# Performance work log

Hardware: AMD Instinct MI355X
Metric: run time of the kernel (lower is better)

Reference implementation:

```python
import math
import jax, jax.numpy as jnp
import numpy as np

CAPACITY_FACTOR = 1.0

def setup_inputs() -> dict:
    key = jax.random.key(0)
    k1, k2 = jax.random.split(key)
    token_input = jax.random.normal(k1, (4096, 1024), dtype=jnp.float32)
    wg2_weight = jax.random.normal(k2, (64, 1024), dtype=jnp.float32) * 0.02
    return {"token_input": token_input, "wg2_weight": wg2_weight}

def reference(token_input, wg2_weight):
    S, _ = token_input.shape
    E = wg2_weight.shape[0]
    num_2nd = E // 4
    capacity = int(2 * math.ceil(S / num_2nd) * CAPACITY_FACTOR)  # static
    eps = jnp.finfo(jnp.float32).eps

    logits = token_input @ wg2_weight.T               # [S, E]
    gates = jax.nn.softmax(logits, axis=-1)           # [S, E]

    # top-1 expert
    idx1 = jnp.argmax(gates, axis=1)                  # [S]
    mask1 = jax.nn.one_hot(idx1, E, dtype=jnp.int32)  # [S, E]

    # second expert via gumbel sampling on the gate values (masked-out top1)
    gumbel = jax.random.gumbel(jax.random.key(42), gates.shape, dtype=jnp.float32)
    noisy = gates + gumbel
    masked = jnp.where(mask1.astype(bool), -jnp.inf, noisy)
    idx2 = jnp.argmax(masked, axis=1)
    mask2 = jax.nn.one_hot(idx2, E, dtype=jnp.int32)

    # cumsum-based slot locations (fused_cumsum_sub_one)
    locations1 = jnp.cumsum(mask1, axis=0) - 1                       # [S, E]
    locations2 = jnp.cumsum(mask2, axis=0) - 1 + jnp.sum(mask1, axis=0, keepdims=True)

    # load-balance aux loss
    me = jnp.mean(gates, axis=0)
    ce = jnp.mean(mask1.astype(gates.dtype), axis=0)
    l_aux = jnp.sum(me * ce) / num_2nd * (E * E)

    # capacity dropping
    mask1 = mask1 * (locations1 < capacity).astype(jnp.int32)
    mask2 = mask2 * (locations2 < capacity).astype(jnp.int32)

    # gate probs renormalized over kept assignments
    gates1_s = jnp.sum(gates * mask1, axis=1)
    gates2_s = jnp.sum(gates * mask2, axis=1)
    denom = jnp.maximum(gates1_s + gates2_s, eps)
    gates1_s = gates1_s / denom
    gates2_s = gates2_s / denom

    loc1_s = jnp.sum(locations1 * mask1, axis=1)      # [S]
    loc2_s = jnp.sum(locations2 * mask2, axis=1)

    gates1 = gates1_s[:, None] * mask1.astype(gates.dtype)  # [S, E]
    gates2 = gates2_s[:, None] * mask2.astype(gates.dtype)

    loc1_sc = jax.nn.one_hot(loc1_s, capacity, dtype=gates.dtype)  # [S, C]
    loc2_sc = jax.nn.one_hot(loc2_s, capacity, dtype=gates.dtype)

    combine_weights = (jnp.einsum('se,sc->sec', gates1, loc1_sc)
                       + jnp.einsum('se,sc->sec', gates2, loc2_sc))  # [S, E, C]
    dispatch_mask = combine_weights > 0
    return l_aux, combine_weights, dispatch_mask
```

## Files before the change

kernel.cpp:

```cpp
#include <hip/hip_runtime.h>
#include <math.h>
#include <stdint.h>

#define S_TOK 4096
#define N_EXP 64
#define MDIM  1024
#define TB    8
#define CAP   512
#define NBLK_GATE (S_TOK / TB)

#define SEC ((size_t)S_TOK * N_EXP * CAP)


struct TokRec { int idx1; int idx2; float g1; float g2; };

__device__ __forceinline__ void tf4(uint32_t& x0, uint32_t& x1,
                                    int r0, int r1, int r2, int r3) {
  x0 += x1; x1 = (x1 << r0) | (x1 >> (32 - r0)); x1 ^= x0;
  x0 += x1; x1 = (x1 << r1) | (x1 >> (32 - r1)); x1 ^= x0;
  x0 += x1; x1 = (x1 << r2) | (x1 >> (32 - r2)); x1 ^= x0;
  x0 += x1; x1 = (x1 << r3) | (x1 >> (32 - r3)); x1 ^= x0;
}

__device__ __forceinline__ float jax_gumbel(uint32_t f) {
  const uint32_t k0 = 0u, k1 = 42u;
  const uint32_t k2 = 0x1BD11BDAu ^ 42u;
  uint32_t x0 = 0u + k0;
  uint32_t x1 = f + k1;
  tf4(x0, x1, 13, 15, 26,  6); x0 += k1; x1 += k2 + 1u;
  tf4(x0, x1, 17, 29, 16, 24); x0 += k2; x1 += k0 + 2u;
  tf4(x0, x1, 13, 15, 26,  6); x0 += k0; x1 += k1 + 3u;
  tf4(x0, x1, 17, 29, 16, 24); x0 += k1; x1 += k2 + 4u;
  tf4(x0, x1, 13, 15, 26,  6); x0 += k2; x1 += k0 + 5u;
  uint32_t bits = x0 ^ x1;
  float u = __uint_as_float((bits >> 9) | 0x3F800000u) - 1.0f;
  u = fmaxf(u, 1.17549435e-38f);
  return -logf(-logf(u));
}

__global__ __launch_bounds__(256) void k_gate(const float* __restrict__ tok,
                                              const float* __restrict__ W,
                                              TokRec* __restrict__ recs,
                                              float* __restrict__ mePart) {
  __shared__ float t_lds[TB * MDIM];
  __shared__ float logits_l[TB * N_EXP];
  __shared__ float meAcc[4][N_EXP];

  const int tid  = threadIdx.x;
  const int wave = tid >> 6;
  const int lane = tid & 63;
  const int tok0 = blockIdx.x * TB;

  {
    const float4* src = (const float4*)(tok + (size_t)tok0 * MDIM);
    float4* dst = (float4*)t_lds;
    #pragma unroll
    for (int i = 0; i < (TB * MDIM / 4) / 256; ++i)
      dst[tid + i * 256] = src[tid + i * 256];
  }
  __syncthreads();

  for (int p = 0; p < N_EXP / 4; ++p) {
    const int e = p * 4 + wave;
    const float* wr = W + (size_t)e * MDIM;
    float acc[TB];
    #pragma unroll
    for (int t = 0; t < TB; ++t) acc[t] = 0.f;
    for (int k = lane; k < MDIM; k += 64) {
      float wv = wr[k];
      #pragma unroll
      for (int t = 0; t < TB; ++t) acc[t] = fmaf(t_lds[t * MDIM + k], wv, acc[t]);
    }
    #pragma unroll
    for (int t = 0; t < TB; ++t) {
      float v = acc[t];
      #pragma unroll
      for (int o = 32; o >= 1; o >>= 1) v += __shfl_xor(v, o, 64);
      if (lane == 0) logits_l[t * N_EXP + e] = v;
    }
  }
  __syncthreads();

  const int e = lane;
  float meLocal = 0.f;
  #pragma unroll
  for (int rep = 0; rep < 2; ++rep) {
    const int t = wave + rep * 4;
    const int s = tok0 + t;
    float x = logits_l[t * N_EXP + e];
    float m = x;
    #pragma unroll
    for (int o = 32; o >= 1; o >>= 1) m = fmaxf(m, __shfl_xor(m, o, 64));
    float ex = expf(x - m);
    float sum = ex;
    #pragma unroll
    for (int o = 32; o >= 1; o >>= 1) sum += __shfl_xor(sum, o, 64);
    float gate = ex / sum;
    meLocal += gate;

    float bv = gate; int bi = e;
    #pragma unroll
    for (int o = 32; o >= 1; o >>= 1) {
      float ov = __shfl_xor(bv, o, 64);
      int   oi = __shfl_xor(bi, o, 64);
      if (ov > bv || (ov == bv && oi < bi)) { bv = ov; bi = oi; }
    }
    const int idx1 = bi;

    float noisy = (e == idx1) ? -INFINITY
                              : (gate + jax_gumbel((uint32_t)(s * N_EXP + e)));
    float bv2 = noisy; int bi2 = e;
    #pragma unroll
    for (int o = 32; o >= 1; o >>= 1) {
      float ov = __shfl_xor(bv2, o, 64);
      int   oi = __shfl_xor(bi2, o, 64);
      if (ov > bv2 || (ov == bv2 && oi < bi2)) { bv2 = ov; bi2 = oi; }
    }
    const int idx2 = bi2;

    float g1 = __shfl(gate, idx1, 64);
    float g2 = __shfl(gate, idx2, 64);
    if (lane == 0) {
      TokRec r; r.idx1 = idx1; r.idx2 = idx2; r.g1 = g1; r.g2 = g2;
      recs[s] = r;
    }
  }
  meAcc[wave][e] = meLocal;
  __syncthreads();
  if (wave == 0)
    mePart[(size_t)blockIdx.x * N_EXP + e] =
        meAcc[0][e] + meAcc[1][e] + meAcc[2][e] + meAcc[3][e];
}

__global__ __launch_bounds__(1024) void k_finish(const TokRec* __restrict__ recs,
                                                 const float* __restrict__ mePart,
                                                 float* __restrict__ out) {
  __shared__ unsigned short pk_l[S_TOK];
  __shared__ unsigned short rank1_l[S_TOK];
  __shared__ unsigned short rank2_l[S_TOK];
  __shared__ int   cnt1[16][N_EXP];
  __shared__ int   cnt2[16][N_EXP];
  __shared__ int   off1[16][N_EXP];
  __shared__ int   off2[16][N_EXP];
  __shared__ int   total1_l[N_EXP];
  __shared__ float meAcc[16][N_EXP];
  __shared__ float laux_l[N_EXP];

  const int tid  = threadIdx.x;
  const int wave = tid >> 6;
  const int lane = tid & 63;

  for (int s = tid; s < S_TOK; s += 1024) {
    TokRec r = recs[s];
    pk_l[s] = (unsigned short)(r.idx1 | (r.idx2 << 8));
  }
  __syncthreads();

  {
    int c1 = 0, c2 = 0;
    const int s0 = wave * (S_TOK / 16);
    for (int j = 0; j < S_TOK / 16; ++j) {
      const int s = s0 + j;
      const int v  = pk_l[s];
      const int v1 = v & 0xFF;
      const int v2 = v >> 8;
      if (v1 == lane) { rank1_l[s] = (unsigned short)c1; ++c1; }
      if (v2 == lane) { rank2_l[s] = (unsigned short)c2; ++c2; }
    }
    cnt1[wave][lane] = c1;
    cnt2[wave][lane] = c2;
  }
  __syncthreads();

  if (tid < N_EXP) {
    int off = 0;
    #pragma unroll
    for (int w = 0; w < 16; ++w) { off1[w][tid] = off; off += cnt1[w][tid]; }
    total1_l[tid] = off;
    int o2 = off;
    #pragma unroll
    for (int w = 0; w < 16; ++w) { off2[w][tid] = o2; o2 += cnt2[w][tid]; }
  }
  __syncthreads();

  float* comb = out + 1;
  float* mask = out + 1 + SEC;
  for (int s = tid; s < S_TOK; s += 1024) {
    TokRec r = recs[s];
    const int w  = s / (S_TOK / 16);
    const int l1 = (int)rank1_l[s] + off1[w][r.idx1];
    const int l2 = (int)rank2_l[s] + off2[w][r.idx2];
    const bool k1 = l1 < CAP;
    const bool k2 = l2 < CAP;
    float g1 = k1 ? r.g1 : 0.f;
    float g2 = k2 ? r.g2 : 0.f;
    float denom = fmaxf(g1 + g2, 1.1920929e-07f);
    float g1n = g1 / denom;
    float g2n = g2 / denom;
    const size_t base = (size_t)s * N_EXP * CAP;
    if (k1) { size_t o = base + (size_t)r.idx1 * CAP + l1; comb[o] = g1n; mask[o] = 1.0f; }
    if (k2) { size_t o = base + (size_t)r.idx2 * CAP + l2; comb[o] = g2n; mask[o] = 1.0f; }
  }

  {
    float a = 0.f;
    for (int b = wave; b < NBLK_GATE; b += 16) a += mePart[(size_t)b * N_EXP + lane];
    meAcc[wave][lane] = a;
  }
  __syncthreads();
  if (tid < N_EXP) {
    float sg = 0.f;
    #pragma unroll
    for (int w = 0; w < 16; ++w) sg += meAcc[w][tid];
    laux_l[tid] = sg * (float)total1_l[tid];
  }
  __syncthreads();
  if (tid == 0) {
    float t = 0.f;
    for (int e2 = 0; e2 < N_EXP; ++e2) t += laux_l[e2];
    out[0] = t * (1.0f / 65536.0f);
  }
}

extern "C" void kernel_launch(void* const* d_in, const int* in_sizes, int n_in,
                              void* d_out, int out_size, void* d_ws, size_t ws_size,
                              hipStream_t stream) {
  const float* tok = (const float*)d_in[0];
  const float* W   = (const float*)d_in[1];
  float* out = (float*)d_out;

  TokRec* recs   = (TokRec*)d_ws;
  float*  mePart = (float*)((char*)d_ws + S_TOK * sizeof(TokRec));

  k_gate  <<<NBLK_GATE, 256, 0, stream>>>(tok, W, recs, mePart);
  k_finish<<<1, 1024, 0, stream>>>(recs, mePart, out);
}
```

Baseline: 1.022 ms.

## Restructure gate GEMV to vectorized direct global loads without LDS staging

The gating matmul no longer stages the token tile in shared memory. Each lane now owns one of 16 experts per wave and one of 4 K-chunks, and reads weights and tokens from global memory as float4 vectors. The cross-lane reduction shrinks from six shuffle steps to two. This removes the LDS copy, the barrier and most shuffle work, but relies on cache broadcast for the token reads, which are repeated across the 16 expert lanes.

```diff
diff --git a/kernel.cpp b/kernel.cpp
--- a/kernel.cpp
+++ b/kernel.cpp
@@ -13,6 +13,8 @@
 
 
 struct TokRec { int idx1; int idx2; float g1; float g2; };
+
+typedef float f4v __attribute__((ext_vector_type(4)));
 
 __device__ __forceinline__ void tf4(uint32_t& x0, uint32_t& x1,
                                     int r0, int r1, int r2, int r3) {
@@ -42,7 +44,6 @@
                                               const float* __restrict__ W,
                                               TokRec* __restrict__ recs,
                                               float* __restrict__ mePart) {
-  __shared__ float t_lds[TB * MDIM];
   __shared__ float logits_l[TB * N_EXP];
   __shared__ float meAcc[4][N_EXP];
 
@@ -51,32 +52,36 @@
   const int lane = tid & 63;
   const int tok0 = blockIdx.x * TB;
 
+  const int e_sub = lane & 15;
+  const int kc    = lane >> 4;
+  const int eW    = wave * 16 + e_sub;
+
   {
-    const float4* src = (const float4*)(tok + (size_t)tok0 * MDIM);
-    float4* dst = (float4*)t_lds;
-    #pragma unroll
-    for (int i = 0; i < (TB * MDIM / 4) / 256; ++i)
-      dst[tid + i * 256] = src[tid + i * 256];
-  }
-  __syncthreads();
-
-  for (int p = 0; p < N_EXP / 4; ++p) {
-    const int e = p * 4 + wave;
-    const float* wr = W + (size_t)e * MDIM;
+    const f4v* wr4 = (const f4v*)(W   + (size_t)eW   * MDIM + kc * 256);
+    const f4v* tp4 = (const f4v*)(tok + (size_t)tok0 * MDIM + kc * 256);
     float acc[TB];
     #pragma unroll
     for (int t = 0; t < TB; ++t) acc[t] = 0.f;
-    for (int k = lane; k < MDIM; k += 64) {
-      float wv = wr[k];
+
+    #pragma unroll 4
+    for (int j = 0; j < 64; ++j) {
+      const f4v wv = wr4[j];
       #pragma unroll
-      for (int t = 0; t < TB; ++t) acc[t] = fmaf(t_lds[t * MDIM + k], wv, acc[t]);
-    }
+      for (int t = 0; t < TB; ++t) {
+        const f4v tv = tp4[t * 256 + j];
+        acc[t] = fmaf(tv.x, wv.x, acc[t]);
+        acc[t] = fmaf(tv.y, wv.y, acc[t]);
+        acc[t] = fmaf(tv.z, wv.z, acc[t]);
+        acc[t] = fmaf(tv.w, wv.w, acc[t]);
+      }
+    }
+
     #pragma unroll
     for (int t = 0; t < TB; ++t) {
       float v = acc[t];
-      #pragma unroll
-      for (int o = 32; o >= 1; o >>= 1) v += __shfl_xor(v, o, 64);
-      if (lane == 0) logits_l[t * N_EXP + e] = v;
+      v += __shfl_xor(v, 16, 64);
+      v += __shfl_xor(v, 32, 64);
+      if (kc == 0) logits_l[t * N_EXP + eW] = v;
     }
   }
   __syncthreads();
```

New measurement: 952.0 us. 6.9% less time.
